# Kernel tuning notes

Hardware: AMD Instinct MI355X
Metric: run time of the kernel (lower is better)

## Reference

```python
import jax, jax.numpy as jnp
import numpy as np

NC, NG, NP = 8192, 4096, 140
FD, D, L = 512, 256, 2
E_OBS, E_COEXP, E_PPI, E_SYM = 300000, 200000, 10000, 20000
EPS = 1e-5


def layer_norm(x, g, b):
    mu = jnp.mean(x, -1, keepdims=True)
    v = jnp.mean((x - mu) ** 2, -1, keepdims=True)
    return (x - mu) * jax.lax.rsqrt(v + EPS) * g + b


def sage(h_src, h_dst, src, dst, w, Ws, Wn, b, n_dst):
    # DGL SAGEConv (mean aggregator, edge-weighted): mean over incoming
    # weighted messages, then fc_self(h_dst) + fc_neigh(neigh) + bias.
    m = h_src[src] * w[:, None]                                  # [E, D]
    neigh = jax.ops.segment_sum(m, dst, num_segments=n_dst)      # [n_dst, D]
    deg = jax.ops.segment_sum(jnp.ones_like(w), dst, num_segments=n_dst)
    neigh = neigh / jnp.maximum(deg, 1.0)[:, None]
    return h_dst @ Ws + neigh @ Wn + b


def setup_inputs() -> dict:
    key = jax.random.key(0)
    ks = iter(jax.random.split(key, 64))
    def n(*s):
        return jax.random.normal(next(ks), s, jnp.float32) * 0.02
    def u(e):
        return jax.random.uniform(next(ks), (e,), jnp.float32)
    def ri(e, hi):
        return jax.random.randint(next(ks), (e,), 0, hi, jnp.int32)
    return dict(
        cell_feat=jax.random.normal(next(ks), (NC, FD), jnp.float32),
        gene_feat=jax.random.normal(next(ks), (NG, FD), jnp.float32),
        pro_idx=jnp.arange(NP, dtype=jnp.int32),
        obs_src=ri(E_OBS, NG), obs_dst=ri(E_OBS, NC), obs_w=u(E_OBS),
        rev_obs_src=ri(E_OBS, NC), rev_obs_dst=ri(E_OBS, NG), rev_obs_w=u(E_OBS),
        symbol_src=ri(E_SYM, NG), symbol_dst=ri(E_SYM, NP), symbol_w=u(E_SYM),
        rev_symbol_src=ri(E_SYM, NP), rev_symbol_dst=ri(E_SYM, NG), rev_symbol_w=u(E_SYM),
        coexp_src=ri(E_COEXP, NG), coexp_dst=ri(E_COEXP, NG), coexp_w=u(E_COEXP),
        ppi_src=ri(E_PPI, NP), ppi_dst=ri(E_PPI, NP), ppi_w=u(E_PPI),
        W_emb_cell=n(FD, D), b_emb_cell=jnp.zeros((D,), jnp.float32),
        W_emb_gene=n(FD, D), b_emb_gene=jnp.zeros((D,), jnp.float32),
        emb_pro=n(NP, D),
        W_mlpcell=n(L, D, D), b_mlpcell=jnp.zeros((L, D), jnp.float32),
        W_sage_self=n(L, 6, D, D), W_sage_neigh=n(L, 6, D, D),
        b_sage=jnp.zeros((L, 6, D), jnp.float32),
        ln1_g=jnp.ones((L, 3, D), jnp.float32), ln1_b=jnp.zeros((L, 3, D), jnp.float32),
        ln2_g=jnp.ones((L, 3, D), jnp.float32), ln2_b=jnp.zeros((L, 3, D), jnp.float32),
        W_last=n(3 * D, NP), b_last=jnp.zeros((NP,), jnp.float32),
    )


def reference(cell_feat, gene_feat, pro_idx,
              obs_src, obs_dst, obs_w,
              rev_obs_src, rev_obs_dst, rev_obs_w,
              symbol_src, symbol_dst, symbol_w,
              rev_symbol_src, rev_symbol_dst, rev_symbol_w,
              coexp_src, coexp_dst, coexp_w,
              ppi_src, ppi_dst, ppi_w,
              W_emb_cell, b_emb_cell, W_emb_gene, b_emb_gene, emb_pro,
              W_mlpcell, b_mlpcell, W_sage_self, W_sage_neigh, b_sage,
              ln1_g, ln1_b, ln2_g, ln2_b, W_last, b_last):
    act = jax.nn.selu
    hc = cell_feat @ W_emb_cell + b_emb_cell      # emb_cell
    hg = gene_feat @ W_emb_gene + b_emb_gene      # emb_gene
    hp = emb_pro[pro_idx]                         # nn.Embedding path
    nc, ng, npn = hc.shape[0], hg.shape[0], hp.shape[0]
    hist = [hc]
    for l in range(W_mlpcell.shape[0]):
        Ws, Wn, bs = W_sage_self[l], W_sage_neigh[l], b_sage[l]
        hmlp = layer_norm(act(hc @ W_mlpcell[l] + b_mlpcell[l]), ln1_g[l, 2], ln1_b[l, 2])
        # HeteroGraphConv(SAGE) over edges_sub = [obs, rev_obs, symbol, rev_symbol] (stack)
        s_obs = sage(hg, hc, obs_src, obs_dst, obs_w, Ws[0], Wn[0], bs[0], nc)
        s_robs = sage(hc, hg, rev_obs_src, rev_obs_dst, rev_obs_w, Ws[1], Wn[1], bs[1], ng)
        s_sym = sage(hg, hp, symbol_src, symbol_dst, symbol_w, Ws[2], Wn[2], bs[2], npn)
        s_rsym = sage(hp, hg, rev_symbol_src, rev_symbol_dst, rev_symbol_w, Ws[3], Wn[3], bs[3], ng)
        # homogeneous subgraph convs: gene_sage on coexp, pro_sage on ppi
        h_gg = layer_norm(act(sage(hg, hg, coexp_src, coexp_dst, coexp_w, Ws[4], Wn[4], bs[4], ng)), ln1_g[l, 0], ln1_b[l, 0])
        h_pp = layer_norm(act(sage(hp, hp, ppi_src, ppi_dst, ppi_w, Ws[5], Wn[5], bs[5], npn)), ln1_g[l, 1], ln1_b[l, 1])
        # norm each stacked relation output, then agg='sum' over the stack dim
        hgen = layer_norm(act(s_robs), ln1_g[l, 0], ln1_b[l, 0]) + layer_norm(act(s_rsym), ln1_g[l, 0], ln1_b[l, 0]) + h_gg
        hpro = layer_norm(act(s_sym), ln1_g[l, 1], ln1_b[l, 1]) + h_pp
        hcel = layer_norm(act(s_obs), ln1_g[l, 2], ln1_b[l, 2]) + hmlp
        hg = layer_norm(act(hgen), ln2_g[l, 0], ln2_b[l, 0])
        hp = layer_norm(act(hpro), ln2_g[l, 1], ln2_b[l, 1])
        hc = layer_norm(act(hcel), ln2_g[l, 2], ln2_b[l, 2])
        hist.append(hc)
    # mlp_last over concat of per-layer cell reps (sum(dims[1:-1]) -> dims[-1])
    return jnp.concatenate(hist, -1) @ W_last + b_last
```

## Files before the change

### kernel.cpp

```cpp
#include <hip/hip_runtime.h>

typedef unsigned short ushort_t;
typedef unsigned int uint_t;

typedef ushort_t ushortx8 __attribute__((ext_vector_type(8)));
typedef ushort_t ushortx4 __attribute__((ext_vector_type(4)));
typedef __bf16 bf16x8 __attribute__((ext_vector_type(8)));
typedef float f32x4 __attribute__((ext_vector_type(4)));

#define NCC 8192
#define NGG 4096
#define NPP 140
#define LDS_STR 88
#define CEPB 16384

__device__ __forceinline__ float bf2f(ushort_t u) {
    uint_t i = ((uint_t)u) << 16;
    float f;
    __builtin_memcpy(&f, &i, 4);
    return f;
}
__device__ __forceinline__ ushort_t f2bf(float f) {
    uint_t i;
    __builtin_memcpy(&i, &f, 4);
    uint_t r = (i + 0x7FFFu + ((i >> 16) & 1u)) >> 16;
    return (ushort_t)r;
}
__device__ __forceinline__ float scrub(float x) {
    return __builtin_isfinite(x) ? x : 0.f;
}
__device__ __forceinline__ float selu_f(float x) {
    return x > 0.f ? 1.0507009873554805f * x : 1.7580993408473766f * expm1f(x);
}
__device__ __forceinline__ float wsum64(float x) {
    for (int o = 32; o; o >>= 1) x += __shfl_xor(x, o, 64);
    return x;
}

__global__ __launch_bounds__(256) void sc_zero1(int* __restrict__ a, int na) {
    int i = blockIdx.x * 256 + threadIdx.x;
    if (i < na) a[i] = 0;
}

struct CountJob {
    const int* dst;
    const int* src;
    const float* w;
    uint_t* pw;
    ushort_t* rank;
    int E;
    int nbins;
    int* deg;
    int bstart;
};
struct CountBatch {
    CountJob j[6];
};
struct TrJob {
    const float* src;
    ushort_t* dst;
    int K, N, nx, nxy;
    int bstart;
};
struct TrBatch {
    TrJob j[6];
};
struct FillJob {
    const int* dst;
    const uint_t* pw;
    const ushort_t* rank;
    int E;
    const int* offs;
    uint_t* ep;
    int bstart;
};
struct FillBatch {
    FillJob j[6];
};

struct CountArgs {
    CountBatch cb;
    int bsC;
    const float* cf;
    ushort_t* cf16;
    int nbC;
    const float* gf;
    ushort_t* gf16;
};
__global__ __launch_bounds__(1024) void sc_count(CountArgs ca) {
    __shared__ int hist[NCC];
    int bx = blockIdx.x;
    const int tid = threadIdx.x;
    if (bx >= ca.bsC) {
        bx -= ca.bsC;
        const float* src;
        ushort_t* dst;
        if (bx < ca.nbC) {
            src = ca.cf;
            dst = ca.cf16;
        } else {
            bx -= ca.nbC;
            src = ca.gf;
            dst = ca.gf16;
        }
        size_t i = ((size_t)bx * 1024 + tid) * 8;
        float4 f0 = *(const float4*)(src + i);
        float4 f1 = *(const float4*)(src + i + 4);
        ushortx8 v;
        v[0] = f2bf(f0.x);
        v[1] = f2bf(f0.y);
        v[2] = f2bf(f0.z);
        v[3] = f2bf(f0.w);
        v[4] = f2bf(f1.x);
        v[5] = f2bf(f1.y);
        v[6] = f2bf(f1.z);
        v[7] = f2bf(f1.w);
        *(ushortx8*)(dst + i) = v;
        return;
    }
    int r = 0;
#pragma unroll
    for (int i = 1; i < 6; ++i) r = (bx >= ca.cb.j[i].bstart) ? i : r;
    const CountJob& J = ca.cb.j[r];
    const int nb = J.nbins;
    const int rep = nb <= 1024 ? 8 : (nb <= 4096 ? 2 : 1);
    const int qoff = (tid & (rep - 1)) * nb;
    const int tot_bins = nb * rep;
    for (int b = tid; b < tot_bins; b += 1024) hist[b] = 0;
    __syncthreads();
    const int e0 = (bx - J.bstart) * CEPB;
    ushort_t lrk[16];
#pragma unroll
    for (int u = 0; u < 16; ++u) {
        int e = e0 + u * 1024 + tid;
        if (e < J.E) {
            int d = J.dst[e];
            lrk[u] = (ushort_t)atomicAdd(&hist[qoff + d], 1);
            J.pw[e] = ((uint_t)f2bf(J.w[e]) << 16) | (uint_t)J.src[e];
        }
    }
    __syncthreads();
    for (int b = tid; b < nb; b += 1024) {
        int c[8];
        int tot = 0;
#pragma unroll
        for (int q = 0; q < 8; ++q) {
            c[q] = (q < rep) ? hist[q * nb + b] : 0;
            tot += c[q];
        }
        if (tot > 0) {
            int run = atomicAdd(&J.deg[b], tot);
#pragma unroll
            for (int q = 0; q < 8; ++q) {
                if (q < rep) {
                    hist[q * nb + b] = run;
                    run += c[q];
                }
            }
        }
    }
    __syncthreads();
#pragma unroll
    for (int u = 0; u < 16; ++u) {
        int e = e0 + u * 1024 + tid;
        if (e < J.E) {
            int d = J.dst[e];
            J.rank[e] = (ushort_t)(hist[qoff + d] + (int)lrk[u]);
        }
    }
}

struct ScanPrepArgs {
    const int* deg_base;
    int* offs_base;
    TrBatch tb;
    int bsT;
    const float* emb;
    const int* pidx;
    ushort_t* hp;
    int nEmb;
};
__global__ __launch_bounds__(1024) void sc_scan_prep(ScanPrepArgs sa) {
    __shared__ int wsum[16];
    __shared__ int carry;
    __shared__ ushort_t tt[32 * 33];
    int bx = blockIdx.x;
    const int tid = threadIdx.x;
    if (bx >= 6) {
        bx -= 6;
        if (bx < sa.bsT) {
            int r = 0;
#pragma unroll
            for (int i = 1; i < 6; ++i) r = (bx >= sa.tb.j[i].bstart) ? i : r;
            const TrJob& J = sa.tb.j[r];
            int local = bx - J.bstart;
            int b = local / J.nxy, rem = local % J.nxy;
            int n0 = (rem % J.nx) * 32, k0 = (rem / J.nx) * 32;
            const float* s = J.src + (size_t)b * J.K * J.N;
            ushort_t* d = J.dst + (size_t)b * J.K * J.N;
            int x = tid & 31, y = tid >> 5;
            {
                int k = k0 + y, n = n0 + x;
                tt[y * 33 + x] =
                    (k < J.K && n < J.N) ? f2bf(s[(size_t)k * J.N + n]) : (ushort_t)0;
            }
            __syncthreads();
            {
                int n = n0 + y, k = k0 + x;
                if (n < J.N && k < J.K) d[(size_t)n * J.K + k] = tt[x * 33 + y];
            }
            return;
        }
        bx -= sa.bsT;
        int i = bx * 1024 + tid;
        if (i < sa.nEmb) {
            int r = i >> 8, c = i & 255;
            int j = sa.pidx[r];
            j = (uint_t)j < (uint_t)NPP ? j : 0;
            sa.hp[i] = f2bf(sa.emb[(size_t)j * 256 + c]);
        }
        return;
    }
    const int ndst[6] = {NCC, NGG, NPP, NGG, NGG, NPP};
    const int dstart[6] = {0, NCC, NCC + NGG, NCC + NGG + NPP, NCC + 2 * NGG + NPP,
                           NCC + 3 * NGG + NPP};
    const int ostart[6] = {0, NCC + 1, NCC + NGG + 2, NCC + NGG + NPP + 3,
                           NCC + 2 * NGG + NPP + 4, NCC + 3 * NGG + NPP + 5};
    int r = bx;
    const int* deg = sa.deg_base + dstart[r];
    int* offs = sa.offs_base + ostart[r];
    int n = ndst[r];
    int wave = tid >> 6, lane = tid & 63;
    if (tid == 0) carry = 0;
    __syncthreads();
    for (int base = 0; base < n; base += 1024) {
        int i = base + tid;
        int v = (i < n) ? deg[i] : 0;
        int x = v;
#pragma unroll
        for (int o = 1; o < 64; o <<= 1) {
            int tv = __shfl_up(x, o, 64);
            if (lane >= o) x += tv;
        }
        if (lane == 63) wsum[wave] = x;
        __syncthreads();
        if (tid == 0) {
            int acc = 0;
#pragma unroll
            for (int k = 0; k < 16; ++k) {
                int tv = wsum[k];
                wsum[k] = acc;
                acc += tv;
            }
        }
        __syncthreads();
        int incl = x + wsum[wave];
        int cr = carry;
        if (i < n) offs[i] = cr + incl - v;
        __syncthreads();
        if (tid == 1023) carry = cr + incl;
        __syncthreads();
    }
    if (tid == 0) offs[n] = carry;
}

struct Emb64Job {
    const ushort_t* A;
    const ushort_t* Bt;
    const float* bias;
    ushort_t* C;
    int ldc;
    ushort_t* C2;
    int mstart;
};
struct FillGemmArgs {
    Emb64Job ej[2];
    int gemmBlocks;
    FillBatch fb;
};
__global__ __launch_bounds__(256) void sc_fill_gemm(FillGemmArgs fg) {
    __shared__ __align__(16) ushort_t As[64 * LDS_STR];
    __shared__ __align__(16) ushort_t Bs[64 * LDS_STR];
    int bx = blockIdx.x;
    if (bx >= fg.gemmBlocks) {
        bx -= fg.gemmBlocks;
        int r = 0;
#pragma unroll
        for (int i = 1; i < 6; ++i) r = (bx >= fg.fb.j[i].bstart) ? i : r;
        const FillJob& J = fg.fb.j[r];
        int e = (bx - J.bstart) * 256 + threadIdx.x;
        if (e < J.E) {
            int d = J.dst[e];
            J.ep[J.offs[d] + (int)J.rank[e]] = J.pw[e];
        }
        return;
    }
    const int mb = bx >> 2, n0 = (bx & 3) * 64;
    const int r = (mb >= fg.ej[1].mstart) ? 1 : 0;
    const Emb64Job& J = fg.ej[r];
    const int m0 = (mb - J.mstart) * 64;
    const ushort_t* A = J.A;
    const ushort_t* Bt = J.Bt;
    const int tid = threadIdx.x;
    const int wave = tid >> 6, lane = tid & 63;
    const int lr = lane & 15, lq = lane >> 4;
    f32x4 acc[4] = {};
    for (int k0 = 0; k0 < 512; k0 += 64) {
        __syncthreads();
#pragma unroll
        for (int i = 0; i < 2; ++i) {
            int g = tid + i * 256;
            int rr = g >> 3, c = (g & 7) * 8;
            *(ushortx8*)(&As[rr * LDS_STR + c]) =
                *(const ushortx8*)(A + (size_t)(m0 + rr) * 512 + k0 + c);
            *(ushortx8*)(&Bs[rr * LDS_STR + c]) =
                *(const ushortx8*)(Bt + (size_t)(n0 + rr) * 512 + k0 + c);
        }
        __syncthreads();
#pragma unroll
        for (int kk = 0; kk < 64; kk += 32) {
            bf16x8 a = __builtin_bit_cast(
                bf16x8, *(const ushortx8*)(&As[(wave * 16 + lr) * LDS_STR + kk + lq * 8]));
            bf16x8 b0 =
                __builtin_bit_cast(bf16x8, *(const ushortx8*)(&Bs[(lr)*LDS_STR + kk + lq * 8]));
            bf16x8 b1 = __builtin_bit_cast(
                bf16x8, *(const ushortx8*)(&Bs[(16 + lr) * LDS_STR + kk + lq * 8]));
            bf16x8 b2 = __builtin_bit_cast(
                bf16x8, *(const ushortx8*)(&Bs[(32 + lr) * LDS_STR + kk + lq * 8]));
            bf16x8 b3 = __builtin_bit_cast(
                bf16x8, *(const ushortx8*)(&Bs[(48 + lr) * LDS_STR + kk + lq * 8]));
            acc[0] = __builtin_amdgcn_mfma_f32_16x16x32_bf16(a, b0, acc[0], 0, 0, 0);
            acc[1] = __builtin_amdgcn_mfma_f32_16x16x32_bf16(a, b1, acc[1], 0, 0, 0);
            acc[2] = __builtin_amdgcn_mfma_f32_16x16x32_bf16(a, b2, acc[2], 0, 0, 0);
            acc[3] = __builtin_amdgcn_mfma_f32_16x16x32_bf16(a, b3, acc[3], 0, 0, 0);
        }
    }
#pragma unroll
    for (int nt = 0; nt < 4; ++nt) {
        int col = n0 + nt * 16 + lr;
        float bb = J.bias[col];
#pragma unroll
        for (int v = 0; v < 4; ++v) {
            int row = m0 + wave * 16 + lq * 4 + v;
            ushort_t val = f2bf(scrub(acc[nt][v] + bb));
            J.C[(size_t)row * J.ldc + col] = val;
            if (J.C2) J.C2[(size_t)row * 256 + col] = val;
        }
    }
}

struct GatherJob {
    const ushort_t* hsrc;
    int src_ld, src_n;
    const int* offs;
    const uint_t* ep;
    ushort_t* out;
    int row_start;
};
struct GatherMlpArgs {
    GatherJob j[6];
    int gemmBlocks;
    const ushort_t* mA;
    const ushort_t* mBt;
    const float* mbias;
    ushort_t* mC;
    int total_rows;
};
__global__ __launch_bounds__(256) void sc_gather_mlp(GatherMlpArgs ga) {
    __shared__ __align__(16) ushort_t As[64 * LDS_STR];
    __shared__ __align__(16) ushort_t Bs[64 * LDS_STR];
    int bx = blockIdx.x;
    const int tid = threadIdx.x;
    if (bx < ga.gemmBlocks) {
        const int mb = bx >> 2, n0 = (bx & 3) * 64;
        const int m0 = mb * 64;
        const int wave = tid >> 6, lane = tid & 63;
        const int lr = lane & 15, lq = lane >> 4;
        f32x4 acc[4] = {};
        for (int k0 = 0; k0 < 256; k0 += 64) {
            __syncthreads();
#pragma unroll
            for (int i = 0; i < 2; ++i) {
                int g = tid + i * 256;
                int rr = g >> 3, c = (g & 7) * 8;
                *(ushortx8*)(&As[rr * LDS_STR + c]) =
                    *(const ushortx8*)(ga.mA + (size_t)(m0 + rr) * 768 + k0 + c);
                *(ushortx8*)(&Bs[rr * LDS_STR + c]) =
                    *(const ushortx8*)(ga.mBt + (size_t)(n0 + rr) * 256 + k0 + c);
            }
            __syncthreads();
#pragma unroll
            for (int kk = 0; kk < 64; kk += 32) {
                bf16x8 a = __builtin_bit_cast(
                    bf16x8, *(const ushortx8*)(&As[(wave * 16 + lr) * LDS_STR + kk + lq * 8]));
                bf16x8 b0 = __builtin_bit_cast(
                    bf16x8, *(const ushortx8*)(&Bs[(lr)*LDS_STR + kk + lq * 8]));
                bf16x8 b1 = __builtin_bit_cast(
                    bf16x8, *(const ushortx8*)(&Bs[(16 + lr) * LDS_STR + kk + lq * 8]));
                bf16x8 b2 = __builtin_bit_cast(
                    bf16x8, *(const ushortx8*)(&Bs[(32 + lr) * LDS_STR + kk + lq * 8]));
                bf16x8 b3 = __builtin_bit_cast(
                    bf16x8, *(const ushortx8*)(&Bs[(48 + lr) * LDS_STR + kk + lq * 8]));
                acc[0] = __builtin_amdgcn_mfma_f32_16x16x32_bf16(a, b0, acc[0], 0, 0, 0);
                acc[1] = __builtin_amdgcn_mfma_f32_16x16x32_bf16(a, b1, acc[1], 0, 0, 0);
                acc[2] = __builtin_amdgcn_mfma_f32_16x16x32_bf16(a, b2, acc[2], 0, 0, 0);
                acc[3] = __builtin_amdgcn_mfma_f32_16x16x32_bf16(a, b3, acc[3], 0, 0, 0);
            }
        }
#pragma unroll
        for (int nt = 0; nt < 4; ++nt) {
            int col = n0 + nt * 16 + lr;
            float bb = ga.mbias[col];
#pragma unroll
            for (int v = 0; v < 4; ++v) {
                int row = m0 + wave * 16 + lq * 4 + v;
                ga.mC[(size_t)row * 256 + col] = f2bf(scrub(acc[nt][v] + bb));
            }
        }
        return;
    }
    bx -= ga.gemmBlocks;
    int grow = bx * 4 + (tid >> 6);
    if (grow >= ga.total_rows) return;
    int r = 0;
#pragma unroll
    for (int i = 1; i < 6; ++i) r = (grow >= ga.j[i].row_start) ? i : r;
    r = __builtin_amdgcn_readfirstlane(r);
    const char* hsrc = (const char*)ga.j[r].hsrc;
    const uint_t row_bytes = (uint_t)(ga.j[r].src_ld * 2);
    const uint_t src_n = (uint_t)ga.j[r].src_n;
    const int* offs = ga.j[r].offs;
    const uint_t* ep = ga.j[r].ep;
    ushort_t* out = ga.j[r].out;
    int row = grow - ga.j[r].row_start;
    int lane = tid & 63;
    int cb = lane * 8;
    int s0 = offs[row], s1 = offs[row + 1];
    float a0 = 0.f, a1 = 0.f, a2 = 0.f, a3 = 0.f;
    for (int base = s0; base < s1; base += 64) {
        int e = base + lane;
        uint_t myp = (e < s1) ? ep[e] : 0u;
        int cnt = s1 - base;
        cnt = cnt < 64 ? cnt : 64;
        int cnt16 = (cnt + 15) & ~15;
        for (int jj = 0; jj < cnt16; jj += 16) {
#pragma unroll
            for (int u = 0; u < 16; ++u) {
                uint_t pw = (uint_t)__builtin_amdgcn_readlane((int)myp, jj + u);
                uint_t s = pw & 0xFFFFu;
                s = s < src_n ? s : 0u;
                float w = bf2f((ushort_t)(pw >> 16));
                const uint2 v = *(const uint2*)(hsrc + (size_t)(s * row_bytes) + cb);
                uint_t x0 = v.x << 16, x1 = v.x & 0xFFFF0000u;
                uint_t x2 = v.y << 16, x3 = v.y & 0xFFFF0000u;
                a0 = fmaf(w, __builtin_bit_cast(float, x0), a0);
                a1 = fmaf(w, __builtin_bit_cast(float, x1), a1);
                a2 = fmaf(w, __builtin_bit_cast(float, x2), a2);
                a3 = fmaf(w, __builtin_bit_cast(float, x3), a3);
            }
        }
    }
    float inv = 1.f / fmaxf((float)(s1 - s0), 1.f);
    ushort_t* o = out + (size_t)row * 256 + lane * 4;
    o[0] = f2bf(scrub(a0 * inv));
    o[1] = f2bf(scrub(a1 * inv));
    o[2] = f2bf(scrub(a2 * inv));
    o[3] = f2bf(scrub(a3 * inv));
}

struct Sage64Job {
    const ushort_t* A1;
    int lda1;
    const ushort_t* Bt1;
    const ushort_t* A2;
    const ushort_t* Bt2;
    const float* bias;
    ushort_t* C;
    int M;
    int mstart;
};
struct Sage64Batch {
    Sage64Job j[6];
};
__global__ __launch_bounds__(256) void sc_gemm_batch64(Sage64Batch gb) {
    __shared__ __align__(16) ushort_t As[64 * LDS_STR];
    __shared__ __align__(16) ushort_t Bs[64 * LDS_STR];
    const int mbx = blockIdx.x, n0 = blockIdx.y * 64;
    int r = 0;
#pragma unroll
    for (int i = 1; i < 6; ++i) r = (mbx >= gb.j[i].mstart) ? i : r;
    const Sage64Job& J = gb.j[r];
    const int m0 = (mbx - J.mstart) * 64;
    const int M = J.M;
    const int tid = threadIdx.x;
    const int wave = tid >> 6, lane = tid & 63;
    const int lr = lane & 15, lq = lane >> 4;
    f32x4 acc[4] = {};
    for (int pass = 0; pass < 2; ++pass) {
        const ushort_t* A = pass ? J.A2 : J.A1;
        const int lda = pass ? 256 : J.lda1;
        const ushort_t* Bt = pass ? J.Bt2 : J.Bt1;
        for (int k0 = 0; k0 < 256; k0 += 64) {
            __syncthreads();
#pragma unroll
            for (int i = 0; i < 2; ++i) {
                int g = tid + i * 256;
                int rr = g >> 3, c = (g & 7) * 8;
                int gm = m0 + rr;
                ushortx8 v = {0, 0, 0, 0, 0, 0, 0, 0};
                if (gm < M) v = *(const ushortx8*)(A + (size_t)gm * lda + k0 + c);
                *(ushortx8*)(&As[rr * LDS_STR + c]) = v;
                *(ushortx8*)(&Bs[rr * LDS_STR + c]) =
                    *(const ushortx8*)(Bt + (size_t)(n0 + rr) * 256 + k0 + c);
            }
            __syncthreads();
#pragma unroll
            for (int kk = 0; kk < 64; kk += 32) {
                bf16x8 a = __builtin_bit_cast(
                    bf16x8, *(const ushortx8*)(&As[(wave * 16 + lr) * LDS_STR + kk + lq * 8]));
                bf16x8 b0 = __builtin_bit_cast(
                    bf16x8, *(const ushortx8*)(&Bs[(lr)*LDS_STR + kk + lq * 8]));
                bf16x8 b1 = __builtin_bit_cast(
                    bf16x8, *(const ushortx8*)(&Bs[(16 + lr) * LDS_STR + kk + lq * 8]));
                bf16x8 b2 = __builtin_bit_cast(
                    bf16x8, *(const ushortx8*)(&Bs[(32 + lr) * LDS_STR + kk + lq * 8]));
                bf16x8 b3 = __builtin_bit_cast(
                    bf16x8, *(const ushortx8*)(&Bs[(48 + lr) * LDS_STR + kk + lq * 8]));
                acc[0] = __builtin_amdgcn_mfma_f32_16x16x32_bf16(a, b0, acc[0], 0, 0, 0);
                acc[1] = __builtin_amdgcn_mfma_f32_16x16x32_bf16(a, b1, acc[1], 0, 0, 0);
                acc[2] = __builtin_amdgcn_mfma_f32_16x16x32_bf16(a, b2, acc[2], 0, 0, 0);
                acc[3] = __builtin_amdgcn_mfma_f32_16x16x32_bf16(a, b3, acc[3], 0, 0, 0);
            }
        }
    }
#pragma unroll
    for (int nt = 0; nt < 4; ++nt) {
        int col = n0 + nt * 16 + lr;
        float bb = J.bias[col];
#pragma unroll
        for (int v = 0; v < 4; ++v) {
            int row = m0 + wave * 16 + lq * 4 + v;
            if (row >= M) continue;
            J.C[(size_t)row * 256 + col] = f2bf(scrub(acc[nt][v] + bb));
        }
    }
}

__global__ __launch_bounds__(256) void sc_gemm(const ushort_t* __restrict__ A1, int lda1,
                                               const ushort_t* __restrict__ Bt1, int K1,
                                               const float* __restrict__ bias,
                                               float* __restrict__ Cf, int ldc, int M, int N) {
    __shared__ __align__(16) ushort_t As[128 * LDS_STR];
    __shared__ __align__(16) ushort_t Bs[64 * LDS_STR];
    const int tid = threadIdx.x;
    const int wave = tid >> 6, lane = tid & 63;
    const int lr = lane & 15, lq = lane >> 4;
    const int m0 = blockIdx.x * 128, n0 = blockIdx.y * 64;
    f32x4 acc[2][4] = {};
    for (int k0 = 0; k0 < K1; k0 += 64) {
        __syncthreads();
#pragma unroll
        for (int i = 0; i < 4; ++i) {
            int g = tid + i * 256;
            int r = g >> 3, c = (g & 7) * 8;
            ushortx8 v = {0, 0, 0, 0, 0, 0, 0, 0};
            int gm = m0 + r;
            if (gm < M) v = *(const ushortx8*)(A1 + (size_t)gm * lda1 + k0 + c);
            *(ushortx8*)(&As[r * LDS_STR + c]) = v;
        }
#pragma unroll
        for (int i = 0; i < 2; ++i) {
            int g = tid + i * 256;
            int r = g >> 3, c = (g & 7) * 8;
            ushortx8 v = {0, 0, 0, 0, 0, 0, 0, 0};
            int gn = n0 + r;
            if (gn < N) v = *(const ushortx8*)(Bt1 + (size_t)gn * K1 + k0 + c);
            *(ushortx8*)(&Bs[r * LDS_STR + c]) = v;
        }
        __syncthreads();
#pragma unroll
        for (int kk = 0; kk < 64; kk += 32) {
            bf16x8 a0 = __builtin_bit_cast(
                bf16x8, *(const ushortx8*)(&As[(wave * 32 + lr) * LDS_STR + kk + lq * 8]));
            bf16x8 a1 = __builtin_bit_cast(
                bf16x8, *(const ushortx8*)(&As[(wave * 32 + 16 + lr) * LDS_STR + kk + lq * 8]));
            bf16x8 b0 =
                __builtin_bit_cast(bf16x8, *(const ushortx8*)(&Bs[(lr)*LDS_STR + kk + lq * 8]));
            bf16x8 b1 = __builtin_bit_cast(
                bf16x8, *(const ushortx8*)(&Bs[(16 + lr) * LDS_STR + kk + lq * 8]));
            bf16x8 b2 = __builtin_bit_cast(
                bf16x8, *(const ushortx8*)(&Bs[(32 + lr) * LDS_STR + kk + lq * 8]));
            bf16x8 b3 = __builtin_bit_cast(
                bf16x8, *(const ushortx8*)(&Bs[(48 + lr) * LDS_STR + kk + lq * 8]));
            acc[0][0] = __builtin_amdgcn_mfma_f32_16x16x32_bf16(a0, b0, acc[0][0], 0, 0, 0);
            acc[0][1] = __builtin_amdgcn_mfma_f32_16x16x32_bf16(a0, b1, acc[0][1], 0, 0, 0);
            acc[0][2] = __builtin_amdgcn_mfma_f32_16x16x32_bf16(a0, b2, acc[0][2], 0, 0, 0);
            acc[0][3] = __builtin_amdgcn_mfma_f32_16x16x32_bf16(a0, b3, acc[0][3], 0, 0, 0);
            acc[1][0] = __builtin_amdgcn_mfma_f32_16x16x32_bf16(a1, b0, acc[1][0], 0, 0, 0);
            acc[1][1] = __builtin_amdgcn_mfma_f32_16x16x32_bf16(a1, b1, acc[1][1], 0, 0, 0);
            acc[1][2] = __builtin_amdgcn_mfma_f32_16x16x32_bf16(a1, b2, acc[1][2], 0, 0, 0);
            acc[1][3] = __builtin_amdgcn_mfma_f32_16x16x32_bf16(a1, b3, acc[1][3], 0, 0, 0);
        }
    }
#pragma unroll
    for (int mt = 0; mt < 2; ++mt)
#pragma unroll
        for (int nt = 0; nt < 4; ++nt) {
            int col = n0 + nt * 16 + lr;
            if (col >= N) continue;
            float bb = bias ? bias[col] : 0.f;
#pragma unroll
            for (int v = 0; v < 4; ++v) {
                int row = m0 + wave * 32 + mt * 16 + lq * 4 + v;
                if (row >= M) continue;
                Cf[(size_t)row * ldc + col] = scrub(acc[mt][nt][v] + bb);
            }
        }
}

struct LnJob {
    const ushort_t *sA, *sB, *sC;
    const float *g1, *b1, *g2, *b2;
    ushort_t* out;
    int out_ld;
    ushort_t* out2;
    int row_start;
};
struct LnBatch {
    LnJob j[3];
};
__global__ __launch_bounds__(256) void sc_fuse_ln_all(LnBatch lb, int total_rows) {
    int grow = blockIdx.x * 4 + (threadIdx.x >> 6);
    if (grow >= total_rows) return;
    int r = 0;
#pragma unroll
    for (int i = 1; i < 3; ++i) r = (grow >= lb.j[i].row_start) ? i : r;
    r = __builtin_amdgcn_readfirstlane(r);
    const ushort_t* srcs[3] = {lb.j[r].sA, lb.j[r].sB, lb.j[r].sC};
    const float* g1 = lb.j[r].g1;
    const float* b1 = lb.j[r].b1;
    const float* g2 = lb.j[r].g2;
    const float* b2 = lb.j[r].b2;
    ushort_t* out = lb.j[r].out;
    int out_ld = lb.j[r].out_ld;
    ushort_t* out2 = lb.j[r].out2;
    int row = grow - lb.j[r].row_start;
    int lane = threadIdx.x & 63, c = lane * 4;
    float t[4] = {0.f, 0.f, 0.f, 0.f};
#pragma unroll
    for (int si = 0; si < 3; ++si) {
        const ushort_t* s = srcs[si];
        if (!s) continue;
        ushortx4 v = *(const ushortx4*)(s + (size_t)row * 256 + c);
        float x0 = selu_f(scrub(bf2f(v[0]))), x1 = selu_f(scrub(bf2f(v[1])));
        float x2 = selu_f(scrub(bf2f(v[2]))), x3 = selu_f(scrub(bf2f(v[3])));
        float mu = wsum64(x0 + x1 + x2 + x3) * (1.f / 256.f);
        float d0 = x0 - mu, d1 = x1 - mu, d2 = x2 - mu, d3 = x3 - mu;
        float var = wsum64(d0 * d0 + d1 * d1 + d2 * d2 + d3 * d3) * (1.f / 256.f);
        float rr = rsqrtf(var + 1e-5f);
        t[0] += d0 * rr * g1[c + 0] + b1[c + 0];
        t[1] += d1 * rr * g1[c + 1] + b1[c + 1];
        t[2] += d2 * rr * g1[c + 2] + b1[c + 2];
        t[3] += d3 * rr * g1[c + 3] + b1[c + 3];
    }
    float x0 = selu_f(scrub(t[0])), x1 = selu_f(scrub(t[1]));
    float x2 = selu_f(scrub(t[2])), x3 = selu_f(scrub(t[3]));
    float mu = wsum64(x0 + x1 + x2 + x3) * (1.f / 256.f);
    float d0 = x0 - mu, d1 = x1 - mu, d2 = x2 - mu, d3 = x3 - mu;
    float var = wsum64(d0 * d0 + d1 * d1 + d2 * d2 + d3 * d3) * (1.f / 256.f);
    float rr = rsqrtf(var + 1e-5f);
    ushort_t o0 = f2bf(scrub(d0 * rr * g2[c + 0] + b2[c + 0]));
    ushort_t o1 = f2bf(scrub(d1 * rr * g2[c + 1] + b2[c + 1]));
    ushort_t o2v = f2bf(scrub(d2 * rr * g2[c + 2] + b2[c + 2]));
    ushort_t o3 = f2bf(scrub(d3 * rr * g2[c + 3] + b2[c + 3]));
    ushort_t* o = out + (size_t)row * out_ld + c;
    o[0] = o0;
    o[1] = o1;
    o[2] = o2v;
    o[3] = o3;
    if (out2) {
        ushort_t* q = out2 + (size_t)row * 256 + c;
        q[0] = o0;
        q[1] = o1;
        q[2] = o2v;
        q[3] = o3;
    }
}

static inline int cdivi(int a, int b) { return (a + b - 1) / b; }

extern "C" void kernel_launch(void* const* d_in, const int* in_sizes, int n_in, void* d_out,
                              int out_size, void* d_ws, size_t ws_size, hipStream_t stream) {
    const float* cell_feat = (const float*)d_in[0];
    const float* gene_feat = (const float*)d_in[1];
    const int* pro_idx = (const int*)d_in[2];
    const int* edge_src[6] = {(const int*)d_in[3],  (const int*)d_in[6],  (const int*)d_in[9],
                              (const int*)d_in[12], (const int*)d_in[15], (const int*)d_in[18]};
    const int* edge_dst[6] = {(const int*)d_in[4],  (const int*)d_in[7],  (const int*)d_in[10],
                              (const int*)d_in[13], (const int*)d_in[16], (const int*)d_in[19]};
    const float* edge_w[6] = {(const float*)d_in[5],  (const float*)d_in[8],
                              (const float*)d_in[11], (const float*)d_in[14],
                              (const float*)d_in[17], (const float*)d_in[20]};
    const float* W_emb_cell = (const float*)d_in[21];
    const float* b_emb_cell = (const float*)d_in[22];
    const float* W_emb_gene = (const float*)d_in[23];
    const float* b_emb_gene = (const float*)d_in[24];
    const float* emb_pro = (const float*)d_in[25];
    const float* W_mlpcell = (const float*)d_in[26];
    const float* b_mlpcell = (const float*)d_in[27];
    const float* W_sage_self = (const float*)d_in[28];
    const float* W_sage_neigh = (const float*)d_in[29];
    const float* b_sage = (const float*)d_in[30];
    const float* ln1_g = (const float*)d_in[31];
    const float* ln1_b = (const float*)d_in[32];
    const float* ln2_g = (const float*)d_in[33];
    const float* ln2_b = (const float*)d_in[34];
    const float* W_last = (const float*)d_in[35];
    const float* b_last = (const float*)d_in[36];

    const int E_obs = in_sizes[3], E_sym = in_sizes[9], E_coexp = in_sizes[15],
              E_ppi = in_sizes[18];
    const int Er[6] = {E_obs, E_obs, E_sym, E_sym, E_coexp, E_ppi};
    const int Nd[6] = {NCC, NGG, NPP, NGG, NGG, NPP};

    char* p = (char*)d_ws;
    auto carve = [&](size_t bytes) -> char* {
        char* r = p;
        p += ((bytes + 255) & ~(size_t)255);
        return r;
    };
    ushort_t* hist = (ushort_t*)carve((size_t)NCC * 768 * 2);
    ushort_t* hg = (ushort_t*)carve((size_t)NGG * 256 * 2);
    ushort_t* hp = (ushort_t*)carve((size_t)NPP * 256 * 2);
    ushort_t* n_obs = (ushort_t*)carve((size_t)NCC * 256 * 2);
    ushort_t* n_robs = (ushort_t*)carve((size_t)NGG * 256 * 2);
    ushort_t* n_sym = (ushort_t*)carve((size_t)NPP * 256 * 2);
    ushort_t* n_rsym = (ushort_t*)carve((size_t)NGG * 256 * 2);
    ushort_t* n_coexp = (ushort_t*)carve((size_t)NGG * 256 * 2);
    ushort_t* n_ppi = (ushort_t*)carve((size_t)NPP * 256 * 2);
    ushort_t* s_obs = (ushort_t*)carve((size_t)NCC * 256 * 2);
    ushort_t* s_robs = (ushort_t*)carve((size_t)NGG * 256 * 2);
    ushort_t* s_sym = (ushort_t*)carve((size_t)NPP * 256 * 2);
    ushort_t* s_rsym = (ushort_t*)carve((size_t)NGG * 256 * 2);
    ushort_t* s_coexp = (ushort_t*)carve((size_t)NGG * 256 * 2);
    ushort_t* s_ppi = (ushort_t*)carve((size_t)NPP * 256 * 2);
    ushort_t* s_mlp = (ushort_t*)carve((size_t)NCC * 256 * 2);
    ushort_t* Wt_emb_cell = (ushort_t*)carve((size_t)512 * 256 * 2);
    ushort_t* Wt_emb_gene = (ushort_t*)carve((size_t)512 * 256 * 2);
    ushort_t* Wt_mlp = (ushort_t*)carve((size_t)2 * 256 * 256 * 2);
    ushort_t* Wt_self = (ushort_t*)carve((size_t)12 * 256 * 256 * 2);
    ushort_t* Wt_neigh = (ushort_t*)carve((size_t)12 * 256 * 256 * 2);
    ushort_t* Wt_last = (ushort_t*)carve((size_t)140 * 768 * 2);
    const int NDTOT = NCC + 3 * NGG + 2 * NPP;
    int* deg_all = (int*)carve((size_t)NDTOT * 4);
    int* offs_all = (int*)carve((size_t)(NDTOT + 6) * 4);
    const int ETOT = 2 * E_obs + 2 * E_sym + E_coexp + E_ppi;
    uint_t* pw_all = (uint_t*)carve((size_t)ETOT * 4);
    ushort_t* rank_all = (ushort_t*)carve((size_t)ETOT * 2);
    uint_t* ep_all = (uint_t*)carve((size_t)ETOT * 4);
    ushort_t* hc_cmp = (ushort_t*)carve((size_t)NCC * 256 * 2);
    ushort_t* cf16 = s_obs;
    ushort_t* gf16 = s_coexp;
    (void)ws_size;
    (void)n_in;
    (void)out_size;

    const int dS[6] = {0, NCC, NCC + NGG, NCC + NGG + NPP, NCC + 2 * NGG + NPP,
                       NCC + 3 * NGG + NPP};
    const int oS[6] = {0, NCC + 1, NCC + NGG + 2, NCC + NGG + NPP + 3, NCC + 2 * NGG + NPP + 4,
                       NCC + 3 * NGG + NPP + 5};
    int eS[6];
    eS[0] = 0;
    eS[1] = eS[0] + E_obs;
    eS[2] = eS[1] + E_obs;
    eS[3] = eS[2] + E_sym;
    eS[4] = eS[3] + E_sym;
    eS[5] = eS[4] + E_coexp;

    sc_zero1<<<cdivi(NDTOT, 256), 256, 0, stream>>>(deg_all, NDTOT);
    {
        CountArgs ca;
        int bs = 0;
        for (int r = 0; r < 6; ++r) {
            ca.cb.j[r] = {edge_dst[r], edge_src[r], edge_w[r], pw_all + eS[r], rank_all + eS[r],
                          Er[r],       Nd[r],       deg_all + dS[r], bs};
            bs += cdivi(Er[r], CEPB);
        }
        ca.bsC = bs;
        ca.cf = cell_feat;
        ca.cf16 = cf16;
        ca.nbC = (NCC * 512) / 8192;
        ca.gf = gene_feat;
        ca.gf16 = gf16;
        int nbG = (NGG * 512) / 8192;
        sc_count<<<bs + ca.nbC + nbG, 1024, 0, stream>>>(ca);
    }
    {
        ScanPrepArgs sa;
        sa.deg_base = deg_all;
        sa.offs_base = offs_all;
        int bt = 0;
        auto add = [&](int idx, const float* s, ushort_t* d, int B, int K, int N) {
            int nx = cdivi(N, 32), ny = cdivi(K, 32);
            sa.tb.j[idx] = {s, d, K, N, nx, nx * ny, bt};
            bt += B * nx * ny;
        };
        add(0, W_emb_cell, Wt_emb_cell, 1, 512, 256);
        add(1, W_emb_gene, Wt_emb_gene, 1, 512, 256);
        add(2, W_mlpcell, Wt_mlp, 2, 256, 256);
        add(3, W_sage_self, Wt_self, 12, 256, 256);
        add(4, W_sage_neigh, Wt_neigh, 12, 256, 256);
        add(5, W_last, Wt_last, 1, 768, 140);
        sa.bsT = bt;
        sa.emb = emb_pro;
        sa.pidx = pro_idx;
        sa.hp = hp;
        sa.nEmb = NPP * 256;
        int bsE = cdivi(NPP * 256, 1024);
        sc_scan_prep<<<6 + bt + bsE, 1024, 0, stream>>>(sa);
    }
    {
        FillGemmArgs fg;
        fg.ej[0] = {cf16, Wt_emb_cell, b_emb_cell, hist, 768, hc_cmp, 0};
        fg.ej[1] = {gf16, Wt_emb_gene, b_emb_gene, hg, 256, nullptr, NCC / 64};
        fg.gemmBlocks = (NCC / 64 + NGG / 64) * 4;
        int bs = 0;
        for (int r = 0; r < 6; ++r) {
            fg.fb.j[r] = {edge_dst[r], pw_all + eS[r], rank_all + eS[r], Er[r], offs_all + oS[r],
                          ep_all + eS[r], bs};
            bs += cdivi(Er[r], 256);
        }
        sc_fill_gemm<<<fg.gemmBlocks + bs, 256, 0, stream>>>(fg);
    }

    for (int l = 0; l < 2; ++l) {
        const ushort_t* hc_l = hist + l * 256;
        {
            GatherMlpArgs ga;
            const ushort_t* hs[6] = {hg, hc_cmp, hg, hp, hg, hp};
            const int sn[6] = {NGG, NCC, NGG, NPP, NGG, NPP};
            ushort_t* outs[6] = {n_obs, n_robs, n_sym, n_rsym, n_coexp, n_ppi};
            int rs = 0;
            for (int r = 0; r < 6; ++r) {
                ga.j[r] = {hs[r], 256, sn[r], offs_all + oS[r], ep_all + eS[r], outs[r], rs};
                rs += Nd[r];
            }
            ga.gemmBlocks = (NCC / 64) * 4;
            ga.mA = hc_l;
            ga.mBt = Wt_mlp + (size_t)l * 65536;
            ga.mbias = b_mlpcell + l * 256;
            ga.mC = s_mlp;
            ga.total_rows = rs;
            sc_gather_mlp<<<ga.gemmBlocks + cdivi(rs, 4), 256, 0, stream>>>(ga);
        }
        {
            const size_t WSZ = 65536;
            Sage64Batch gb;
            const ushort_t* dstf[6] = {hc_l, hg, hp, hg, hg, hp};
            const int dld[6] = {768, 256, 256, 256, 256, 256};
            const ushort_t* nb[6] = {n_obs, n_robs, n_sym, n_rsym, n_coexp, n_ppi};
            ushort_t* so[6] = {s_obs, s_robs, s_sym, s_rsym, s_coexp, s_ppi};
            int ms = 0;
            for (int r = 0; r < 6; ++r) {
                gb.j[r] = {dstf[r],
                           dld[r],
                           Wt_self + (size_t)(l * 6 + r) * WSZ,
                           nb[r],
                           Wt_neigh + (size_t)(l * 6 + r) * WSZ,
                           b_sage + (l * 6 + r) * 256,
                           so[r],
                           Nd[r],
                           ms};
                ms += cdivi(Nd[r], 64);
            }
            sc_gemm_batch64<<<dim3(ms, 4), 256, 0, stream>>>(gb);
        }
        {
            LnBatch lb;
            lb.j[0] = {s_robs, s_rsym, s_coexp, ln1_g + (l * 3 + 0) * 256,
                       ln1_b + (l * 3 + 0) * 256, ln2_g + (l * 3 + 0) * 256,
                       ln2_b + (l * 3 + 0) * 256, hg, 256, nullptr, 0};
            lb.j[1] = {s_sym, s_ppi, nullptr, ln1_g + (l * 3 + 1) * 256,
                       ln1_b + (l * 3 + 1) * 256, ln2_g + (l * 3 + 1) * 256,
                       ln2_b + (l * 3 + 1) * 256, hp, 256, nullptr, NGG};
            lb.j[2] = {s_obs, s_mlp, nullptr, ln1_g + (l * 3 + 2) * 256,
                       ln1_b + (l * 3 + 2) * 256, ln2_g + (l * 3 + 2) * 256,
                       ln2_b + (l * 3 + 2) * 256, hist + (l + 1) * 256, 768,
                       (l == 0) ? hc_cmp : nullptr, NGG + NPP};
            int rs = NGG + NPP + NCC;
            sc_fuse_ln_all<<<cdivi(rs, 4), 256, 0, stream>>>(lb, rs);
        }
    }

    sc_gemm<<<dim3(64, 3), 256, 0, stream>>>(hist, 768, Wt_last, 768, b_last, (float*)d_out, 140,
                                             NCC, 140);
}
```

Measured before the change: 370.5 us.

## Move self-term SAGE GEMMs into the gather kernel and interleave GEMM and gather blocks

The h_dst@Ws + bias part of every SAGE relation now runs inside the gather/MLP kernel alongside the neighbour gathers, because it does not depend on the aggregated neighbours. Block indices are spread evenly between GEMM and gather work so compute-bound and memory-bound blocks run together. The later kernel then only does neigh@Wn and accumulates into the existing output, halving its K loop. The cost is a read-modify-write of the output in bf16, which adds an extra rounding step, plus extra job-dispatch logic.

```diff
diff --git a/kernel.cpp b/kernel.cpp
--- a/kernel.cpp
+++ b/kernel.cpp
@@ -357,23 +357,39 @@
     ushort_t* out;
     int row_start;
 };
+struct GMJob {
+    const ushort_t* A;
+    int lda;
+    const ushort_t* Bt;
+    const float* bias;
+    ushort_t* C;
+    int M;
+    int mstart;
+};
 struct GatherMlpArgs {
     GatherJob j[6];
+    GMJob g[7];
     int gemmBlocks;
-    const ushort_t* mA;
-    const ushort_t* mBt;
-    const float* mbias;
-    ushort_t* mC;
+    int totalBlocks;
     int total_rows;
 };
 __global__ __launch_bounds__(256) void sc_gather_mlp(GatherMlpArgs ga) {
     __shared__ __align__(16) ushort_t As[64 * LDS_STR];
     __shared__ __align__(16) ushort_t Bs[64 * LDS_STR];
-    int bx = blockIdx.x;
+    const int bx = blockIdx.x;
     const int tid = threadIdx.x;
-    if (bx < ga.gemmBlocks) {
-        const int mb = bx >> 2, n0 = (bx & 3) * 64;
-        const int m0 = mb * 64;
+    const long long G = ga.gemmBlocks, T = ga.totalBlocks;
+    const int prev = (int)(((long long)bx * G) / T);
+    const int nxt = (int)(((long long)(bx + 1) * G) / T);
+    if (nxt > prev) {
+        const int gb = prev;
+        const int mb = gb >> 2, n0 = (gb & 3) * 64;
+        int r = 0;
+#pragma unroll
+        for (int i = 1; i < 7; ++i) r = (mb >= ga.g[i].mstart) ? i : r;
+        const GMJob& J = ga.g[r];
+        const int m0 = (mb - J.mstart) * 64;
+        const int M = J.M;
         const int wave = tid >> 6, lane = tid & 63;
         const int lr = lane & 15, lq = lane >> 4;
         f32x4 acc[4] = {};
@@ -383,10 +399,12 @@
             for (int i = 0; i < 2; ++i) {
                 int g = tid + i * 256;
                 int rr = g >> 3, c = (g & 7) * 8;
-                *(ushortx8*)(&As[rr * LDS_STR + c]) =
-                    *(const ushortx8*)(ga.mA + (size_t)(m0 + rr) * 768 + k0 + c);
+                int gm = m0 + rr;
+                ushortx8 v = {0, 0, 0, 0, 0, 0, 0, 0};
+                if (gm < M) v = *(const ushortx8*)(J.A + (size_t)gm * J.lda + k0 + c);
+                *(ushortx8*)(&As[rr * LDS_STR + c]) = v;
                 *(ushortx8*)(&Bs[rr * LDS_STR + c]) =
-                    *(const ushortx8*)(ga.mBt + (size_t)(n0 + rr) * 256 + k0 + c);
+                    *(const ushortx8*)(J.Bt + (size_t)(n0 + rr) * 256 + k0 + c);
             }
             __syncthreads();
 #pragma unroll
@@ -410,17 +428,17 @@
 #pragma unroll
         for (int nt = 0; nt < 4; ++nt) {
             int col = n0 + nt * 16 + lr;
-            float bb = ga.mbias[col];
+            float bb = J.bias[col];
 #pragma unroll
             for (int v = 0; v < 4; ++v) {
                 int row = m0 + wave * 16 + lq * 4 + v;
-                ga.mC[(size_t)row * 256 + col] = f2bf(scrub(acc[nt][v] + bb));
+                if (row >= M) continue;
+                J.C[(size_t)row * 256 + col] = f2bf(scrub(acc[nt][v] + bb));
             }
         }
         return;
     }
-    bx -= ga.gemmBlocks;
-    int grow = bx * 4 + (tid >> 6);
+    int grow = (bx - prev) * 4 + (tid >> 6);
     if (grow >= ga.total_rows) return;
     int r = 0;
 #pragma unroll
@@ -468,80 +486,71 @@
     o[3] = f2bf(scrub(a3 * inv));
 }
 
-struct Sage64Job {
-    const ushort_t* A1;
-    int lda1;
-    const ushort_t* Bt1;
-    const ushort_t* A2;
-    const ushort_t* Bt2;
-    const float* bias;
+struct NeighJob {
+    const ushort_t* A;
+    const ushort_t* Bt;
     ushort_t* C;
     int M;
     int mstart;
 };
-struct Sage64Batch {
-    Sage64Job j[6];
-};
-__global__ __launch_bounds__(256) void sc_gemm_batch64(Sage64Batch gb) {
+struct NeighBatch {
+    NeighJob j[6];
+};
+__global__ __launch_bounds__(256) void sc_gemm_neigh(NeighBatch gb) {
     __shared__ __align__(16) ushort_t As[64 * LDS_STR];
     __shared__ __align__(16) ushort_t Bs[64 * LDS_STR];
     const int mbx = blockIdx.x, n0 = blockIdx.y * 64;
     int r = 0;
 #pragma unroll
     for (int i = 1; i < 6; ++i) r = (mbx >= gb.j[i].mstart) ? i : r;
-    const Sage64Job& J = gb.j[r];
+    const NeighJob& J = gb.j[r];
     const int m0 = (mbx - J.mstart) * 64;
     const int M = J.M;
     const int tid = threadIdx.x;
     const int wave = tid >> 6, lane = tid & 63;
     const int lr = lane & 15, lq = lane >> 4;
     f32x4 acc[4] = {};
-    for (int pass = 0; pass < 2; ++pass) {
-        const ushort_t* A = pass ? J.A2 : J.A1;
-        const int lda = pass ? 256 : J.lda1;
-        const ushort_t* Bt = pass ? J.Bt2 : J.Bt1;
-        for (int k0 = 0; k0 < 256; k0 += 64) {
-            __syncthreads();
-#pragma unroll
-            for (int i = 0; i < 2; ++i) {
-                int g = tid + i * 256;
-                int rr = g >> 3, c = (g & 7) * 8;
-                int gm = m0 + rr;
-                ushortx8 v = {0, 0, 0, 0, 0, 0, 0, 0};
-                if (gm < M) v = *(const ushortx8*)(A + (size_t)gm * lda + k0 + c);
-                *(ushortx8*)(&As[rr * LDS_STR + c]) = v;
-                *(ushortx8*)(&Bs[rr * LDS_STR + c]) =
-                    *(const ushortx8*)(Bt + (size_t)(n0 + rr) * 256 + k0 + c);
-            }
-            __syncthreads();
-#pragma unroll
-            for (int kk = 0; kk < 64; kk += 32) {
-                bf16x8 a = __builtin_bit_cast(
-                    bf16x8, *(const ushortx8*)(&As[(wave * 16 + lr) * LDS_STR + kk + lq * 8]));
-                bf16x8 b0 = __builtin_bit_cast(
-                    bf16x8, *(const ushortx8*)(&Bs[(lr)*LDS_STR + kk + lq * 8]));
-                bf16x8 b1 = __builtin_bit_cast(
-                    bf16x8, *(const ushortx8*)(&Bs[(16 + lr) * LDS_STR + kk + lq * 8]));
-                bf16x8 b2 = __builtin_bit_cast(
-                    bf16x8, *(const ushortx8*)(&Bs[(32 + lr) * LDS_STR + kk + lq * 8]));
-                bf16x8 b3 = __builtin_bit_cast(
-                    bf16x8, *(const ushortx8*)(&Bs[(48 + lr) * LDS_STR + kk + lq * 8]));
-                acc[0] = __builtin_amdgcn_mfma_f32_16x16x32_bf16(a, b0, acc[0], 0, 0, 0);
-                acc[1] = __builtin_amdgcn_mfma_f32_16x16x32_bf16(a, b1, acc[1], 0, 0, 0);
-                acc[2] = __builtin_amdgcn_mfma_f32_16x16x32_bf16(a, b2, acc[2], 0, 0, 0);
-                acc[3] = __builtin_amdgcn_mfma_f32_16x16x32_bf16(a, b3, acc[3], 0, 0, 0);
-            }
+    for (int k0 = 0; k0 < 256; k0 += 64) {
+        __syncthreads();
+#pragma unroll
+        for (int i = 0; i < 2; ++i) {
+            int g = tid + i * 256;
+            int rr = g >> 3, c = (g & 7) * 8;
+            int gm = m0 + rr;
+            ushortx8 v = {0, 0, 0, 0, 0, 0, 0, 0};
+            if (gm < M) v = *(const ushortx8*)(J.A + (size_t)gm * 256 + k0 + c);
+            *(ushortx8*)(&As[rr * LDS_STR + c]) = v;
+            *(ushortx8*)(&Bs[rr * LDS_STR + c]) =
+                *(const ushortx8*)(J.Bt + (size_t)(n0 + rr) * 256 + k0 + c);
+        }
+        __syncthreads();
+#pragma unroll
+        for (int kk = 0; kk < 64; kk += 32) {
+            bf16x8 a = __builtin_bit_cast(
+                bf16x8, *(const ushortx8*)(&As[(wave * 16 + lr) * LDS_STR + kk + lq * 8]));
+            bf16x8 b0 =
+                __builtin_bit_cast(bf16x8, *(const ushortx8*)(&Bs[(lr)*LDS_STR + kk + lq * 8]));
+            bf16x8 b1 = __builtin_bit_cast(
+                bf16x8, *(const ushortx8*)(&Bs[(16 + lr) * LDS_STR + kk + lq * 8]));
+            bf16x8 b2 = __builtin_bit_cast(
+                bf16x8, *(const ushortx8*)(&Bs[(32 + lr) * LDS_STR + kk + lq * 8]));
+            bf16x8 b3 = __builtin_bit_cast(
+                bf16x8, *(const ushortx8*)(&Bs[(48 + lr) * LDS_STR + kk + lq * 8]));
+            acc[0] = __builtin_amdgcn_mfma_f32_16x16x32_bf16(a, b0, acc[0], 0, 0, 0);
+            acc[1] = __builtin_amdgcn_mfma_f32_16x16x32_bf16(a, b1, acc[1], 0, 0, 0);
+            acc[2] = __builtin_amdgcn_mfma_f32_16x16x32_bf16(a, b2, acc[2], 0, 0, 0);
+            acc[3] = __builtin_amdgcn_mfma_f32_16x16x32_bf16(a, b3, acc[3], 0, 0, 0);
         }
     }
 #pragma unroll
     for (int nt = 0; nt < 4; ++nt) {
         int col = n0 + nt * 16 + lr;
-        float bb = J.bias[col];
 #pragma unroll
         for (int v = 0; v < 4; ++v) {
             int row = m0 + wave * 16 + lq * 4 + v;
             if (row >= M) continue;
-            J.C[(size_t)row * 256 + col] = f2bf(scrub(acc[nt][v] + bb));
+            size_t idx = (size_t)row * 256 + col;
+            J.C[idx] = f2bf(scrub(bf2f(J.C[idx]) + acc[nt][v]));
         }
     }
 }
@@ -833,47 +842,49 @@
         sc_fill_gemm<<<fg.gemmBlocks + bs, 256, 0, stream>>>(fg);
     }
 
+    const size_t WSZ = 65536;
     for (int l = 0; l < 2; ++l) {
         const ushort_t* hc_l = hist + l * 256;
+        const ushort_t* dstf[6] = {hc_l, hg, hp, hg, hg, hp};
+        const int dld[6] = {768, 256, 256, 256, 256, 256};
+        const ushort_t* nbuf[6] = {n_obs, n_robs, n_sym, n_rsym, n_coexp, n_ppi};
+        ushort_t* so[6] = {s_obs, s_robs, s_sym, s_rsym, s_coexp, s_ppi};
         {
             GatherMlpArgs ga;
             const ushort_t* hs[6] = {hg, hc_cmp, hg, hp, hg, hp};
             const int sn[6] = {NGG, NCC, NGG, NPP, NGG, NPP};
-            ushort_t* outs[6] = {n_obs, n_robs, n_sym, n_rsym, n_coexp, n_ppi};
             int rs = 0;
             for (int r = 0; r < 6; ++r) {
-                ga.j[r] = {hs[r], 256, sn[r], offs_all + oS[r], ep_all + eS[r], outs[r], rs};
+                ga.j[r] = {hs[r], 256, sn[r], offs_all + oS[r], ep_all + eS[r],
+                           (ushort_t*)nbuf[r], rs};
                 rs += Nd[r];
             }
-            ga.gemmBlocks = (NCC / 64) * 4;
-            ga.mA = hc_l;
-            ga.mBt = Wt_mlp + (size_t)l * 65536;
-            ga.mbias = b_mlpcell + l * 256;
-            ga.mC = s_mlp;
+            ga.g[0] = {hc_l, 768, Wt_mlp + (size_t)l * WSZ, b_mlpcell + l * 256, s_mlp, NCC, 0};
+            int msg = NCC / 64;
+            for (int r = 0; r < 6; ++r) {
+                ga.g[r + 1] = {dstf[r],
+                               dld[r],
+                               Wt_self + (size_t)(l * 6 + r) * WSZ,
+                               b_sage + (l * 6 + r) * 256,
+                               so[r],
+                               Nd[r],
+                               msg};
+                msg += cdivi(Nd[r], 64);
+            }
+            ga.gemmBlocks = msg * 4;
+            int gBlocks = cdivi(rs, 4);
+            ga.totalBlocks = ga.gemmBlocks + gBlocks;
             ga.total_rows = rs;
-            sc_gather_mlp<<<ga.gemmBlocks + cdivi(rs, 4), 256, 0, stream>>>(ga);
+            sc_gather_mlp<<<ga.totalBlocks, 256, 0, stream>>>(ga);
         }
         {
-            const size_t WSZ = 65536;
-            Sage64Batch gb;
-            const ushort_t* dstf[6] = {hc_l, hg, hp, hg, hg, hp};
-            const int dld[6] = {768, 256, 256, 256, 256, 256};
-            const ushort_t* nb[6] = {n_obs, n_robs, n_sym, n_rsym, n_coexp, n_ppi};
-            ushort_t* so[6] = {s_obs, s_robs, s_sym, s_rsym, s_coexp, s_ppi};
+            NeighBatch nb;
             int ms = 0;
             for (int r = 0; r < 6; ++r) {
-                gb.j[r] = {dstf[r],
-                           dld[r],
-                           Wt_self + (size_t)(l * 6 + r) * WSZ,
-                           nb[r],
-                           Wt_neigh + (size_t)(l * 6 + r) * WSZ,
-                           b_sage + (l * 6 + r) * 256,
-                           so[r],
-                           Nd[r],
-                           ms};
+                nb.j[r] = {nbuf[r], Wt_neigh + (size_t)(l * 6 + r) * WSZ, so[r], Nd[r], ms};
                 ms += cdivi(Nd[r], 64);
             }
-            sc_gemm_batch64<<<dim3(ms, 4), 256, 0, stream>>>(gb);
+            sc_gemm_neigh<<<dim3(ms, 4), 256, 0, stream>>>(nb);
         }
         {
             LnBatch lb;
```

Measured after the change: 377.3 us. About the same (+1.8%).
